# Performance work log

Measured on AMD Instinct MI355X. Metric: run time of the kernel, lower is better.

## Reference

```python
import jax, jax.numpy as jnp
import numpy as np

DIM, HEADS, MLP_HID = 1024, 16, 4096
B, N = 2, 2048
EPS = 1e-5

def setup_inputs() -> dict:
    key = jax.random.key(0)
    ks = jax.random.split(key, 8)
    s = lambda fan_in: 1.0 / np.sqrt(fan_in)
    return {
        "x": jax.random.normal(ks[0], (B, N, DIM), jnp.float32),
        "ln1_w": jnp.ones((DIM,), jnp.float32),
        "ln1_b": jnp.zeros((DIM,), jnp.float32),
        # weights stored [in, out] (transpose of torch Linear.weight)
        "qkv_w": jax.random.normal(ks[1], (DIM, 3 * DIM), jnp.float32) * s(DIM),
        "proj_w": jax.random.normal(ks[2], (DIM, DIM), jnp.float32) * s(DIM),
        "proj_b": jnp.zeros((DIM,), jnp.float32),
        "ln2_w": jnp.ones((DIM,), jnp.float32),
        "ln2_b": jnp.zeros((DIM,), jnp.float32),
        "fc1_w": jax.random.normal(ks[3], (DIM, MLP_HID), jnp.float32) * s(DIM),
        "fc1_b": jnp.zeros((MLP_HID,), jnp.float32),
        "fc2_w": jax.random.normal(ks[4], (MLP_HID, DIM), jnp.float32) * s(MLP_HID),
        "fc2_b": jnp.zeros((DIM,), jnp.float32),
    }

def _layernorm(x, w, b):
    mu = jnp.mean(x, axis=-1, keepdims=True)
    var = jnp.mean(jnp.square(x - mu), axis=-1, keepdims=True)
    return (x - mu) * jax.lax.rsqrt(var + EPS) * w + b

def reference(x, ln1_w, ln1_b, qkv_w, proj_w, proj_b, ln2_w, ln2_b, fc1_w, fc1_b, fc2_w, fc2_b):
    Bn, Nn, C = x.shape
    H, D = HEADS, C // HEADS
    scale = D ** -0.5

    # --- attention sub-block (pre-norm, residual) ---
    h = _layernorm(x, ln1_w, ln1_b)
    qkv = (h @ qkv_w).reshape(Bn, Nn, 3, H, D)
    q, k, v = jnp.moveaxis(qkv, 2, 0)  # each [B, N, H, D]
    attn = jnp.einsum('bnhd,bmhd->bhnm', q, k) * scale
    attn = jax.nn.softmax(attn, axis=-1)
    o = jnp.einsum('bhnm,bmhd->bnhd', attn, v).reshape(Bn, Nn, C)
    x = x + (o @ proj_w + proj_b)

    # --- MLP sub-block (pre-norm, residual) ---
    h = _layernorm(x, ln2_w, ln2_b)
    h = jax.nn.gelu(h @ fc1_w + fc1_b, approximate=False)
    x = x + (h @ fc2_w + fc2_b)
    return x
```

## Files before the change

### kernel.cpp

```cpp
#include <hip/hip_runtime.h>
#include <hip/hip_bf16.h>

typedef __attribute__((ext_vector_type(4))) float  f32x4;
typedef __attribute__((ext_vector_type(8))) short  short8;
typedef __attribute__((ext_vector_type(8))) unsigned short ushort8;
typedef __attribute__((ext_vector_type(4))) unsigned short u16x4;
typedef unsigned short u16;

__device__ __forceinline__ u16 f2bf(float f) {
    unsigned int u = __builtin_bit_cast(unsigned int, f);
    return (u16)((u + 0x7fffu + ((u >> 16) & 1u)) >> 16);
}

__device__ __forceinline__ unsigned cvtpk(float lo, float hi) {
    unsigned r;
    asm("v_cvt_pk_bf16_f32 %0, %1, %2" : "=v"(r) : "v"(lo), "v"(hi));
    return r;
}

__device__ __forceinline__ f32x4 mfma16(short8 a, short8 b, f32x4 c) {
    return __builtin_amdgcn_mfma_f32_16x16x32_bf16(a, b, c, 0, 0, 0);
}

__device__ __forceinline__ float fexp2(float x) {
    float r;
    asm("v_exp_f32 %0, %1" : "=v"(r) : "v"(x));
    return r;
}

__device__ __forceinline__ float fgelu(float v) {
    const float t = v * v;
    const float u = v * (-2.302118f - 0.102944f * t);
    return v / (1.0f + fexp2(u));
}

__device__ __forceinline__ void gload_lds16(const u16* g, u16* l) {
    __builtin_amdgcn_global_load_lds(
        (__attribute__((address_space(1))) void*)(uintptr_t)(g),
        (__attribute__((address_space(3))) void*)(unsigned)(uintptr_t)(l),
        16, 0, 0);
}

__device__ __forceinline__ void tcast_body(const float* __restrict__ W,
                                           u16* __restrict__ Wt,
                                           int K, int N, int bx, int by) {
    __shared__ float tile[32][33];
    const int tx = threadIdx.x & 31, ty = threadIdx.x >> 5;
    const int c0 = bx * 32;
    const int r0 = by * 32;
#pragma unroll
    for (int i = 0; i < 32; i += 8)
        tile[ty + i][tx] = W[(size_t)(r0 + ty + i) * N + c0 + tx];
    __syncthreads();
#pragma unroll
    for (int i = 0; i < 32; i += 8)
        Wt[(size_t)(c0 + ty + i) * K + r0 + tx] = f2bf(tile[tx][ty + i]);
}

__device__ __forceinline__ void ln_body(const float* __restrict__ x,
                                        const float* __restrict__ w,
                                        const float* __restrict__ b,
                                        u16* __restrict__ out, int row) {
    const int tid = threadIdx.x;
    const float4 v = ((const float4*)(x + (size_t)row * 1024))[tid];
    float s1 = v.x + v.y + v.z + v.w;
    float s2 = v.x * v.x + v.y * v.y + v.z * v.z + v.w * v.w;
#pragma unroll
    for (int m = 1; m < 64; m <<= 1) { s1 += __shfl_xor(s1, m); s2 += __shfl_xor(s2, m); }
    __shared__ float red1[4], red2[4];
    const int wave = tid >> 6, lane = tid & 63;
    if (lane == 0) { red1[wave] = s1; red2[wave] = s2; }
    __syncthreads();
    s1 = red1[0] + red1[1] + red1[2] + red1[3];
    s2 = red2[0] + red2[1] + red2[2] + red2[3];
    const float mean = s1 * (1.0f / 1024.0f);
    const float var  = s2 * (1.0f / 1024.0f) - mean * mean;
    const float rstd = rsqrtf(var + 1e-5f);
    const float4 wv = ((const float4*)w)[tid];
    const float4 bv = ((const float4*)b)[tid];
    u16x4 o;
    o[0] = f2bf((v.x - mean) * rstd * wv.x + bv.x);
    o[1] = f2bf((v.y - mean) * rstd * wv.y + bv.y);
    o[2] = f2bf((v.z - mean) * rstd * wv.z + bv.z);
    o[3] = f2bf((v.w - mean) * rstd * wv.w + bv.w);
    *(u16x4*)(out + (size_t)row * 1024 + tid * 4) = o;
}

__global__ __launch_bounds__(256) void prep1_kernel(const float* __restrict__ x,
                                                    const float* __restrict__ ln1w,
                                                    const float* __restrict__ ln1b,
                                                    u16* __restrict__ h1,
                                                    const float* __restrict__ qkvw,
                                                    u16* __restrict__ wt_qkv) {
    int id = blockIdx.x;
    if (id < 4096) { ln_body(x, ln1w, ln1b, h1, id); return; }
    id -= 4096;
    tcast_body(qkvw, wt_qkv, 1024, 3072, id % 96, id / 96);
}

__global__ __launch_bounds__(256) void ln_kernel(const float* __restrict__ x,
                                                 const float* __restrict__ w,
                                                 const float* __restrict__ b,
                                                 u16* __restrict__ out) {
    ln_body(x, w, b, out, blockIdx.x);
}

__device__ __forceinline__ void tcast_body512(const float* __restrict__ W,
                                              u16* __restrict__ Wt,
                                              int K, int N, int bx, int by,
                                              float (*tile)[33]) {
    const int tx = threadIdx.x & 31, ty = threadIdx.x >> 5;
    const int c0 = bx * 32;
    const int r0 = by * 32;
#pragma unroll
    for (int i = 0; i < 32; i += 16)
        tile[ty + i][tx] = W[(size_t)(r0 + ty + i) * N + c0 + tx];
    __syncthreads();
#pragma unroll
    for (int i = 0; i < 32; i += 16)
        Wt[(size_t)(c0 + ty + i) * K + r0 + tx] = f2bf(tile[tx][ty + i]);
}

__global__ __launch_bounds__(512, 2) void qkvfused_kernel(const u16* __restrict__ A,
                                                          const u16* __restrict__ Bt,
                                                          u16* __restrict__ Cout,
                                                          const float* __restrict__ projw,
                                                          u16* __restrict__ wt_proj,
                                                          const float* __restrict__ fc1w,
                                                          u16* __restrict__ wt_fc1,
                                                          const float* __restrict__ fc2w,
                                                          u16* __restrict__ wt_fc2) {
    __shared__ __align__(16) u16 Ag[3][256 * 32];
    __shared__ __align__(16) u16 Bg[3][128 * 32];
    __shared__ float tile[32][33];
    constexpr int K = 1024, N = 3072;

    if (blockIdx.x >= 384) {
        int id = blockIdx.x - 384;
        if (id < 1024) { tcast_body512(projw, wt_proj, 1024, 1024, id % 32, id / 32, tile); return; }
        id -= 1024;
        if (id < 4096) { tcast_body512(fc1w, wt_fc1, 1024, 4096, id % 128, id / 128, tile); return; }
        id -= 4096;
        tcast_body512(fc2w, wt_fc2, 4096, 1024, id % 32, id / 32, tile);
        return;
    }

    const int tid = threadIdx.x;
    const int wave = tid >> 6, lane = tid & 63;
    const int wr = wave >> 2, wc = wave & 3;
    const int fq = lane >> 4, fr = lane & 15;

    int bid = blockIdx.x;
    bid = (bid & 7) * 48 + (bid >> 3);
    const size_t bm = (size_t)(bid / 24) * 256, bn = (size_t)(bid % 24) * 128;

    const int ko = (fq ^ ((fr >> 1) & 3)) * 8;

    const int srow = tid >> 2;
    const int scol = ((tid & 3) ^ ((tid >> 3) & 3)) * 8;
    const u16* Asrc = A  + (bm + srow) * (size_t)K + scol;
    const u16* Bsrc = Bt + (bn + srow) * (size_t)K + scol;
    const int sdst = wave * 512;

    f32x4 acc[8][2] = {};

    auto STAGE_G = [&](int slot, int kc) {
        gload_lds16(Asrc + kc,                      &Ag[slot][sdst]);
        gload_lds16(Asrc + (size_t)128 * K + kc,    &Ag[slot][sdst + 4096]);
        gload_lds16(Bsrc + kc,                      &Bg[slot][sdst]);
    };

    const int NG = K >> 5;
    STAGE_G(0, 0); STAGE_G(1, 32);
    asm volatile("s_waitcnt vmcnt(3)" ::: "memory");
    __builtin_amdgcn_s_barrier();

    int slot = 0;
    for (int g = 0; g < NG; g++) {
        short8 bfr[2], af[4];
#pragma unroll
        for (int nt = 0; nt < 2; nt++)
            bfr[nt] = *(const short8*)&Bg[slot][(wc * 32 + nt * 16 + fr) * 32 + ko];
#pragma unroll
        for (int m2 = 0; m2 < 4; m2++)
            af[m2] = *(const short8*)&Ag[slot][(wr * 128 + m2 * 16 + fr) * 32 + ko];
        if (g + 2 < NG) {
            const int s2 = slot >= 1 ? slot - 1 : slot + 2;
            STAGE_G(s2, (g + 2) * 32);
        }
        __builtin_amdgcn_s_barrier();
        __builtin_amdgcn_s_setprio(1);
#pragma unroll
        for (int m2 = 0; m2 < 4; m2++)
#pragma unroll
            for (int nt = 0; nt < 2; nt++)
                acc[m2][nt] = mfma16(af[m2], bfr[nt], acc[m2][nt]);
        __builtin_amdgcn_s_setprio(0);
        __builtin_amdgcn_s_barrier();
#pragma unroll
        for (int m2 = 0; m2 < 4; m2++)
            af[m2] = *(const short8*)&Ag[slot][(wr * 128 + (m2 + 4) * 16 + fr) * 32 + ko];
        __builtin_amdgcn_s_barrier();
        __builtin_amdgcn_s_setprio(1);
#pragma unroll
        for (int m2 = 0; m2 < 4; m2++)
#pragma unroll
            for (int nt = 0; nt < 2; nt++)
                acc[m2 + 4][nt] = mfma16(af[m2], bfr[nt], acc[m2 + 4][nt]);
        __builtin_amdgcn_s_setprio(0);
        if (g < NG - 2) { asm volatile("s_waitcnt vmcnt(3)" ::: "memory"); }
        else            { asm volatile("s_waitcnt vmcnt(0)" ::: "memory"); }
        __builtin_amdgcn_s_barrier();
        slot = slot == 2 ? 0 : slot + 1;
    }
#pragma unroll
    for (int mt = 0; mt < 8; mt++) {
#pragma unroll
        for (int nt = 0; nt < 2; nt++) {
            const size_t col = bn + wc * 32 + nt * 16 + fr;
#pragma unroll
            for (int j = 0; j < 4; j++) {
                const size_t row = bm + wr * 128 + mt * 16 + fq * 4 + j;
                Cout[row * N + col] = f2bf(acc[mt][nt][j]);
            }
        }
    }
}

template <int HAS_BIAS, int HAS_RES, int DO_GELU, int OUT_BF16>
__global__ __launch_bounds__(512, 2) void gemm8_kernel(const u16* __restrict__ A,
                                                       const u16* __restrict__ Bt,
                                                       const float* __restrict__ bias,
                                                       const float* __restrict__ res,
                                                       void* __restrict__ Cout,
                                                       int M, int N, int K) {
    __shared__ __align__(16) u16 Ag[3][256 * 32];
    __shared__ __align__(16) u16 Bg[3][128 * 32];
    const int tid = threadIdx.x;
    const int wave = tid >> 6, lane = tid & 63;
    const int wr = wave >> 2, wc = wave & 3;
    const int fq = lane >> 4, fr = lane & 15;

    const int gx = gridDim.x;
    const int nwg = gx * gridDim.y;
    int bid = blockIdx.y * gx + blockIdx.x;
    bid = (bid & 7) * (nwg >> 3) + (bid >> 3);
    const size_t bm = (size_t)(bid / gx) * 256, bn = (size_t)(bid % gx) * 128;

    const int ko = (fq ^ ((fr >> 1) & 3)) * 8;

    const int srow = tid >> 2;
    const int scol = ((tid & 3) ^ ((tid >> 3) & 3)) * 8;
    const u16* Asrc = A  + (bm + srow) * (size_t)K + scol;
    const u16* Bsrc = Bt + (bn + srow) * (size_t)K + scol;
    const int sdst = wave * 512;

    f32x4 acc[8][2] = {};

    auto STAGE_G = [&](int slot, int kc) {
        gload_lds16(Asrc + kc,                      &Ag[slot][sdst]);
        gload_lds16(Asrc + (size_t)128 * K + kc,    &Ag[slot][sdst + 4096]);
        gload_lds16(Bsrc + kc,                      &Bg[slot][sdst]);
    };

    const int NG = K >> 5;
    STAGE_G(0, 0); STAGE_G(1, 32);
    asm volatile("s_waitcnt vmcnt(3)" ::: "memory");
    __builtin_amdgcn_s_barrier();

    int slot = 0;
    for (int g = 0; g < NG; g++) {
        short8 bfr[2], af[4];
#pragma unroll
        for (int nt = 0; nt < 2; nt++)
            bfr[nt] = *(const short8*)&Bg[slot][(wc * 32 + nt * 16 + fr) * 32 + ko];
#pragma unroll
        for (int m2 = 0; m2 < 4; m2++)
            af[m2] = *(const short8*)&Ag[slot][(wr * 128 + m2 * 16 + fr) * 32 + ko];
        if (g + 2 < NG) {
            const int s2 = slot >= 1 ? slot - 1 : slot + 2;
            STAGE_G(s2, (g + 2) * 32);
        }
        __builtin_amdgcn_s_barrier();
        __builtin_amdgcn_s_setprio(1);
#pragma unroll
        for (int m2 = 0; m2 < 4; m2++)
#pragma unroll
            for (int nt = 0; nt < 2; nt++)
                acc[m2][nt] = mfma16(af[m2], bfr[nt], acc[m2][nt]);
        __builtin_amdgcn_s_setprio(0);
        __builtin_amdgcn_s_barrier();
#pragma unroll
        for (int m2 = 0; m2 < 4; m2++)
            af[m2] = *(const short8*)&Ag[slot][(wr * 128 + (m2 + 4) * 16 + fr) * 32 + ko];
        __builtin_amdgcn_s_barrier();
        __builtin_amdgcn_s_setprio(1);
#pragma unroll
        for (int m2 = 0; m2 < 4; m2++)
#pragma unroll
            for (int nt = 0; nt < 2; nt++)
                acc[m2 + 4][nt] = mfma16(af[m2], bfr[nt], acc[m2 + 4][nt]);
        __builtin_amdgcn_s_setprio(0);
        if (g < NG - 2) { asm volatile("s_waitcnt vmcnt(3)" ::: "memory"); }
        else            { asm volatile("s_waitcnt vmcnt(0)" ::: "memory"); }
        __builtin_amdgcn_s_barrier();
        slot = slot == 2 ? 0 : slot + 1;
    }
#pragma unroll
    for (int mt = 0; mt < 8; mt++) {
#pragma unroll
        for (int nt = 0; nt < 2; nt++) {
            const size_t col = bn + wc * 32 + nt * 16 + fr;
            const float bb = HAS_BIAS ? bias[col] : 0.0f;
#pragma unroll
            for (int j = 0; j < 4; j++) {
                const size_t row = bm + wr * 128 + mt * 16 + fq * 4 + j;
                float v = acc[mt][nt][j] + bb;
                if (DO_GELU) v = fgelu(v);
                if (HAS_RES) v += res[row * N + col];
                if (OUT_BF16) ((u16*)Cout)[row * N + col] = f2bf(v);
                else          ((float*)Cout)[row * N + col] = v;
            }
        }
    }
}

template <int HAS_BIAS, int HAS_RES, int DO_GELU, int OUT_BF16>
__global__ __launch_bounds__(256) void gemm64_kernel(const u16* __restrict__ A,
                                                     const u16* __restrict__ Bt,
                                                     const float* __restrict__ bias,
                                                     const float* __restrict__ res,
                                                     void* __restrict__ Cout,
                                                     int M, int N, int K) {
    __shared__ __align__(16) u16 As[2][64 * 64];
    __shared__ __align__(16) u16 Bs[2][128 * 64];
    const int tid = threadIdx.x;
    const int wave = tid >> 6, lane = tid & 63;
    const int wc = wave;
    const int fq = lane >> 4, fr = lane & 15;

    const int gx = gridDim.x;
    const int nwg = gx * gridDim.y;
    int bid = blockIdx.y * gx + blockIdx.x;
    bid = (bid & 7) * (nwg >> 3) + (bid >> 3);
    const size_t bm = (size_t)(bid / gx) * 64, bn = (size_t)(bid % gx) * 128;

    const int lr = lane >> 3, seg = lane & 7;
    const int seg2 = seg ^ lr;

    const u16* Ab = A  + bm * (size_t)K + seg2 * 8;
    const u16* Bb = Bt + bn * (size_t)K + seg2 * 8;

    const int rx = fr & 7;
    const int ko0 = ((0 + fq) ^ rx) * 8;
    const int ko1 = ((4 + fq) ^ rx) * 8;

    f32x4 acc[4][2] = {};

    auto STAGE = [&](int buf, int k0) {
#pragma unroll
        for (int s = 0; s < 2; s++)
            gload_lds16(Ab + (size_t)(s * 32 + wave * 8 + lr) * K + k0,
                        &As[buf][s * 2048 + wave * 512]);
#pragma unroll
        for (int s = 0; s < 4; s++)
            gload_lds16(Bb + (size_t)(s * 32 + wave * 8 + lr) * K + k0,
                        &Bs[buf][s * 2048 + wave * 512]);
    };

    STAGE(0, 0);
    __syncthreads();
    int cur = 0;

    for (int k0 = 0; k0 < K; k0 += 64) {
        if (k0 + 64 < K) STAGE(cur ^ 1, k0 + 64);
#pragma unroll
        for (int ks = 0; ks < 2; ks++) {
            const int ko = ks ? ko1 : ko0;
            short8 af[4], bf[2];
#pragma unroll
            for (int t = 0; t < 4; t++)
                af[t] = *(const short8*)&As[cur][(t * 16 + fr) * 64 + ko];
#pragma unroll
            for (int nt = 0; nt < 2; nt++)
                bf[nt] = *(const short8*)&Bs[cur][(wc * 32 + nt * 16 + fr) * 64 + ko];
#pragma unroll
            for (int mt = 0; mt < 4; mt++)
#pragma unroll
                for (int nt = 0; nt < 2; nt++)
                    acc[mt][nt] = mfma16(af[mt], bf[nt], acc[mt][nt]);
        }
        __syncthreads();
        cur ^= 1;
    }
#pragma unroll
    for (int mt = 0; mt < 4; mt++) {
#pragma unroll
        for (int nt = 0; nt < 2; nt++) {
            const size_t col = bn + wc * 32 + nt * 16 + fr;
            const float bb = HAS_BIAS ? bias[col] : 0.0f;
#pragma unroll
            for (int j = 0; j < 4; j++) {
                const size_t row = bm + mt * 16 + fq * 4 + j;
                float v = acc[mt][nt][j] + bb;
                if (DO_GELU) v = fgelu(v);
                if (HAS_RES) v += res[row * N + col];
                if (OUT_BF16) ((u16*)Cout)[row * N + col] = f2bf(v);
                else          ((float*)Cout)[row * N + col] = v;
            }
        }
    }
}

__global__ __launch_bounds__(512) void attn_kernel(const u16* __restrict__ qkv,
                                                   u16* __restrict__ O) {
    const int bh = blockIdx.x;
    const int b = bh >> 4, h = bh & 15;
    const int qb = blockIdx.y;
    const int tid = threadIdx.x, wave = tid >> 6, lane = tid & 63;
    const int fq = lane >> 4, fr = lane & 15;
    __shared__ __align__(16) u16 Ks[2][64 * 64];
    __shared__ __align__(16) u16 Vt[2][64 * 64];
    __shared__ __align__(16) u16 Pl[8][16 * 64];

    const size_t base = (size_t)b * 2048 * 3072;
    const int q0 = qb * 128 + wave * 16;

    short8 qf[2];
#pragma unroll
    for (int ks = 0; ks < 2; ks++)
        qf[ks] = *(const short8*)(qkv + base + (size_t)(q0 + fr) * 3072 + h * 64 + ks * 32 + fq * 8);

    const u16* kp = qkv + base + 1024 + (size_t)h * 64;
    const u16* vp = qkv + base + 2048 + (size_t)h * 64;
    const int krow = tid >> 3, kseg = tid & 7;
    const int kpos = (kseg ^ (krow & 7)) * 8;
    const int vkey = tid & 63, vdc = tid >> 6;

    const int rx = fr & 7;
    const int ko0 = ((0 + fq) ^ rx) * 8;
    const int ko1 = ((4 + fq) ^ rx) * 8;

    f32x4 accO[4] = {};
    float lq = 0.0f;

    const float c = 0.125f * 1.44269504f;

    ushort8 kreg = *(const ushort8*)(kp + (size_t)krow * 3072 + kseg * 8);
    ushort8 vreg = *(const ushort8*)(vp + (size_t)vkey * 3072 + vdc * 8);
    *(ushort8*)&Ks[0][krow * 64 + kpos] = kreg;
#pragma unroll
    for (int j = 0; j < 8; j++) {
        const int row = vdc * 8 + j;
        Vt[0][row * 64 + ((vkey >> 3) ^ (row & 7)) * 8 + (vkey & 7)] = vreg[j];
    }
    __syncthreads();
    int cur = 0;

    for (int kt = 0; kt < 32; kt++) {
        if (kt < 31) {
            kreg = *(const ushort8*)(kp + (size_t)((kt + 1) * 64 + krow) * 3072 + kseg * 8);
            vreg = *(const ushort8*)(vp + (size_t)((kt + 1) * 64 + vkey) * 3072 + vdc * 8);
        }
        f32x4 s[4];
#pragma unroll
        for (int nt = 0; nt < 4; nt++) {
            f32x4 a = {};
            short8 kf0 = *(const short8*)&Ks[cur][(nt * 16 + fr) * 64 + ko0];
            short8 kf1 = *(const short8*)&Ks[cur][(nt * 16 + fr) * 64 + ko1];
            a = mfma16(kf0, qf[0], a);
            a = mfma16(kf1, qf[1], a);
            s[nt] = a;
        }
#pragma unroll
        for (int nt = 0; nt < 4; nt++)
#pragma unroll
            for (int j = 0; j < 4; j++) {
                const float pij = fexp2(s[nt][j] * c);
                s[nt][j] = pij;
                lq += pij;
            }
#pragma unroll
        for (int nt = 0; nt < 4; nt++) {
            uint2 pw;
            pw.x = cvtpk(s[nt][0], s[nt][1]);
            pw.y = cvtpk(s[nt][2], s[nt][3]);
            const int chunk = nt * 2 + (fq >> 1);
            *(uint2*)&Pl[wave][fr * 64 + (chunk ^ rx) * 8 + (fq & 1) * 4] = pw;
        }
#pragma unroll
        for (int ks = 0; ks < 2; ks++) {
            const int ko = ks ? ko1 : ko0;
            short8 pf = *(const short8*)&Pl[wave][fr * 64 + ko];
#pragma unroll
            for (int dt = 0; dt < 4; dt++) {
                short8 vf = *(const short8*)&Vt[cur][(dt * 16 + fr) * 64 + ko];
                accO[dt] = mfma16(pf, vf, accO[dt]);
            }
        }
        if (kt < 31) {
            *(ushort8*)&Ks[cur ^ 1][krow * 64 + kpos] = kreg;
#pragma unroll
            for (int j = 0; j < 8; j++) {
                const int row = vdc * 8 + j;
                Vt[cur ^ 1][row * 64 + ((vkey >> 3) ^ (row & 7)) * 8 + (vkey & 7)] = vreg[j];
            }
        }
        __syncthreads();
        cur ^= 1;
    }
    lq += __shfl_xor(lq, 16);
    lq += __shfl_xor(lq, 32);
    float rq[4];
#pragma unroll
    for (int j = 0; j < 4; j++) rq[j] = 1.0f / __shfl(lq, fq * 4 + j);
#pragma unroll
    for (int dt = 0; dt < 4; dt++)
#pragma unroll
        for (int j = 0; j < 4; j++) {
            const float v = accO[dt][j] * rq[j];
            O[(size_t)(b * 2048 + q0 + fq * 4 + j) * 1024 + h * 64 + dt * 16 + fr] = f2bf(v);
        }
}

extern "C" void kernel_launch(void* const* d_in, const int* in_sizes, int n_in,
                              void* d_out, int out_size, void* d_ws, size_t ws_size,
                              hipStream_t stream) {
    (void)in_sizes; (void)n_in; (void)out_size; (void)ws_size;
    const float* x     = (const float*)d_in[0];
    const float* ln1w  = (const float*)d_in[1];
    const float* ln1b  = (const float*)d_in[2];
    const float* qkvw  = (const float*)d_in[3];
    const float* projw = (const float*)d_in[4];
    const float* projb = (const float*)d_in[5];
    const float* ln2w  = (const float*)d_in[6];
    const float* ln2b  = (const float*)d_in[7];
    const float* fc1w  = (const float*)d_in[8];
    const float* fc1b  = (const float*)d_in[9];
    const float* fc2w  = (const float*)d_in[10];
    const float* fc2b  = (const float*)d_in[11];

    char* p = (char*)d_ws;
    auto alloc = [&](size_t bytes) { void* r = p; p += (bytes + 255) & ~(size_t)255; return r; };
    u16* wt_qkv  = (u16*)alloc(3072ull * 1024 * 2);
    u16* wt_proj = (u16*)alloc(1024ull * 1024 * 2);
    u16* wt_fc1  = (u16*)alloc(4096ull * 1024 * 2);
    u16* wt_fc2  = (u16*)alloc(1024ull * 4096 * 2);
    u16* h1      = (u16*)alloc(4096ull * 1024 * 2);
    u16* qkv     = (u16*)alloc(4096ull * 3072 * 2);
    u16* attn_o  = (u16*)alloc(4096ull * 1024 * 2);
    u16* h2      = (u16*)alloc(4096ull * 1024 * 2);
    u16* mlp_h   = (u16*)alloc(4096ull * 4096 * 2);
    float* x1 = (float*)d_out;

    prep1_kernel<<<7168, 256, 0, stream>>>(x, ln1w, ln1b, h1, qkvw, wt_qkv);

    qkvfused_kernel<<<9600, 512, 0, stream>>>(h1, wt_qkv, qkv,
                                              projw, wt_proj, fc1w, wt_fc1, fc2w, wt_fc2);

    attn_kernel<<<dim3(32, 16), 512, 0, stream>>>(qkv, attn_o);
    gemm64_kernel<1, 1, 0, 0><<<dim3(8, 64), 256, 0, stream>>>(attn_o, wt_proj, projb, x, x1, 4096, 1024, 1024);

    ln_kernel<<<4096, 256, 0, stream>>>(x1, ln2w, ln2b, h2);
    gemm8_kernel<1, 0, 1, 1><<<dim3(32, 16), 512, 0, stream>>>(h2, wt_fc1, fc1b, nullptr, mlp_h, 4096, 4096, 1024);
    gemm64_kernel<1, 1, 0, 0><<<dim3(8, 64), 256, 0, stream>>>(mlp_h, wt_fc2, fc2b, x1, d_out, 4096, 1024, 4096);
}
```

Measured before the change: 210.5 us.

## Write V transposed from QKV GEMM and stage K/V via direct global-to-LDS loads

The QKV GEMM epilogue now writes the V third of its output transposed into a separate [B, C, N] buffer. This lets the attention kernel stage both K and V tiles with direct global-to-LDS 16-byte loads instead of register loads followed by scattered per-element transposing LDS stores. The goal is to remove the costly V transpose scatter and the register staging from the attention inner loop. In exchange the GEMM epilogue does strided 8-byte stores into the transposed buffer, and an extra 8 MB workspace is used.

```diff
diff --git a/kernel.cpp b/kernel.cpp
--- a/kernel.cpp
+++ b/kernel.cpp
@@ -124,6 +124,7 @@
 __global__ __launch_bounds__(512, 2) void qkvfused_kernel(const u16* __restrict__ A,
                                                           const u16* __restrict__ Bt,
                                                           u16* __restrict__ Cout,
+                                                          u16* __restrict__ vt,
                                                           const float* __restrict__ projw,
                                                           u16* __restrict__ wt_proj,
                                                           const float* __restrict__ fc1w,
@@ -213,15 +214,31 @@
         __builtin_amdgcn_s_barrier();
         slot = slot == 2 ? 0 : slot + 1;
     }
-#pragma unroll
-    for (int mt = 0; mt < 8; mt++) {
-#pragma unroll
-        for (int nt = 0; nt < 2; nt++) {
-            const size_t col = bn + wc * 32 + nt * 16 + fr;
-#pragma unroll
-            for (int j = 0; j < 4; j++) {
-                const size_t row = bm + wr * 128 + mt * 16 + fq * 4 + j;
-                Cout[row * N + col] = f2bf(acc[mt][nt][j]);
+    if (bn >= 2048) {
+#pragma unroll
+        for (int mt = 0; mt < 8; mt++) {
+#pragma unroll
+            for (int nt = 0; nt < 2; nt++) {
+                const size_t col = (bn - 2048) + wc * 32 + nt * 16 + fr;
+                const size_t row = bm + wr * 128 + mt * 16 + fq * 4;
+                const size_t n = row & 2047, bb = row >> 11;
+                u16x4 pw;
+#pragma unroll
+                for (int j = 0; j < 4; j++) pw[j] = f2bf(acc[mt][nt][j]);
+                *(u16x4*)&vt[(bb * 1024 + col) * 2048 + n] = pw;
+            }
+        }
+    } else {
+#pragma unroll
+        for (int mt = 0; mt < 8; mt++) {
+#pragma unroll
+            for (int nt = 0; nt < 2; nt++) {
+                const size_t col = bn + wc * 32 + nt * 16 + fr;
+#pragma unroll
+                for (int j = 0; j < 4; j++) {
+                    const size_t row = bm + wr * 128 + mt * 16 + fq * 4 + j;
+                    Cout[row * N + col] = f2bf(acc[mt][nt][j]);
+                }
             }
         }
     }
@@ -413,6 +430,7 @@
 }
 
 __global__ __launch_bounds__(512) void attn_kernel(const u16* __restrict__ qkv,
+                                                   const u16* __restrict__ vt,
                                                    u16* __restrict__ O) {
     const int bh = blockIdx.x;
     const int b = bh >> 4, h = bh & 15;
@@ -420,7 +438,7 @@
     const int tid = threadIdx.x, wave = tid >> 6, lane = tid & 63;
     const int fq = lane >> 4, fr = lane & 15;
     __shared__ __align__(16) u16 Ks[2][64 * 64];
-    __shared__ __align__(16) u16 Vt[2][64 * 64];
+    __shared__ __align__(16) u16 Vs[2][64 * 64];
     __shared__ __align__(16) u16 Pl[8][16 * 64];
 
     const size_t base = (size_t)b * 2048 * 3072;
@@ -431,11 +449,11 @@
     for (int ks = 0; ks < 2; ks++)
         qf[ks] = *(const short8*)(qkv + base + (size_t)(q0 + fr) * 3072 + h * 64 + ks * 32 + fq * 8);
 
-    const u16* kp = qkv + base + 1024 + (size_t)h * 64;
-    const u16* vp = qkv + base + 2048 + (size_t)h * 64;
-    const int krow = tid >> 3, kseg = tid & 7;
-    const int kpos = (kseg ^ (krow & 7)) * 8;
-    const int vkey = tid & 63, vdc = tid >> 6;
+    const int srow = tid >> 3, schunk = tid & 7;
+    const int spos = (schunk ^ (srow & 7)) * 8;
+    const u16* kdma = qkv + base + 1024 + (size_t)h * 64 + (size_t)srow * 3072 + spos;
+    const u16* vdma = vt + ((size_t)b * 1024 + h * 64 + srow) * 2048 + spos;
+    const int sdst = wave * 512;
 
     const int rx = fr & 7;
     const int ko0 = ((0 + fq) ^ rx) * 8;
@@ -446,22 +464,17 @@
 
     const float c = 0.125f * 1.44269504f;
 
-    ushort8 kreg = *(const ushort8*)(kp + (size_t)krow * 3072 + kseg * 8);
-    ushort8 vreg = *(const ushort8*)(vp + (size_t)vkey * 3072 + vdc * 8);
-    *(ushort8*)&Ks[0][krow * 64 + kpos] = kreg;
-#pragma unroll
-    for (int j = 0; j < 8; j++) {
-        const int row = vdc * 8 + j;
-        Vt[0][row * 64 + ((vkey >> 3) ^ (row & 7)) * 8 + (vkey & 7)] = vreg[j];
-    }
+    auto STAGE = [&](int buf, int kt) {
+        gload_lds16(kdma + (size_t)kt * 64 * 3072, &Ks[buf][sdst]);
+        gload_lds16(vdma + kt * 64,                &Vs[buf][sdst]);
+    };
+
+    STAGE(0, 0);
     __syncthreads();
     int cur = 0;
 
     for (int kt = 0; kt < 32; kt++) {
-        if (kt < 31) {
-            kreg = *(const ushort8*)(kp + (size_t)((kt + 1) * 64 + krow) * 3072 + kseg * 8);
-            vreg = *(const ushort8*)(vp + (size_t)((kt + 1) * 64 + vkey) * 3072 + vdc * 8);
-        }
+        if (kt < 31) STAGE(cur ^ 1, kt + 1);
         f32x4 s[4];
 #pragma unroll
         for (int nt = 0; nt < 4; nt++) {
@@ -494,16 +507,8 @@
             short8 pf = *(const short8*)&Pl[wave][fr * 64 + ko];
 #pragma unroll
             for (int dt = 0; dt < 4; dt++) {
-                short8 vf = *(const short8*)&Vt[cur][(dt * 16 + fr) * 64 + ko];
+                short8 vf = *(const short8*)&Vs[cur][(dt * 16 + fr) * 64 + ko];
                 accO[dt] = mfma16(pf, vf, accO[dt]);
-            }
-        }
-        if (kt < 31) {
-            *(ushort8*)&Ks[cur ^ 1][krow * 64 + kpos] = kreg;
-#pragma unroll
-            for (int j = 0; j < 8; j++) {
-                const int row = vdc * 8 + j;
-                Vt[cur ^ 1][row * 64 + ((vkey >> 3) ^ (row & 7)) * 8 + (vkey & 7)] = vreg[j];
             }
         }
         __syncthreads();
@@ -548,6 +553,7 @@
     u16* wt_fc2  = (u16*)alloc(1024ull * 4096 * 2);
     u16* h1      = (u16*)alloc(4096ull * 1024 * 2);
     u16* qkv     = (u16*)alloc(4096ull * 3072 * 2);
+    u16* vt      = (u16*)alloc(2048ull * 2048 * 2);
     u16* attn_o  = (u16*)alloc(4096ull * 1024 * 2);
     u16* h2      = (u16*)alloc(4096ull * 1024 * 2);
     u16* mlp_h   = (u16*)alloc(4096ull * 4096 * 2);
@@ -555,10 +561,10 @@
 
     prep1_kernel<<<7168, 256, 0, stream>>>(x, ln1w, ln1b, h1, qkvw, wt_qkv);
 
-    qkvfused_kernel<<<9600, 512, 0, stream>>>(h1, wt_qkv, qkv,
+    qkvfused_kernel<<<9600, 512, 0, stream>>>(h1, wt_qkv, qkv, vt,
                                               projw, wt_proj, fc1w, wt_fc1, fc2w, wt_fc2);
 
-    attn_kernel<<<dim3(32, 16), 512, 0, stream>>>(qkv, attn_o);
+    attn_kernel<<<dim3(32, 16), 512, 0, stream>>>(qkv, vt, attn_o);
     gemm64_kernel<1, 1, 0, 0><<<dim3(8, 64), 256, 0, stream>>>(attn_o, wt_proj, projb, x, x1, 4096, 1024, 1024);
 
     ln_kernel<<<4096, 256, 0, stream>>>(x1, ln2w, ln2b, h2);
```

Result: slower. 222.0 us (+5.5%).
